# Kernel optimization log

Measured on AMD Instinct MI355X. Metric: run time of the kernel, lower is better.

The kernel has to match this reference:

```python
import jax, jax.numpy as jnp
import numpy as np

BS = 16
CIN = 32          # input_channels
COUT = 64         # out_channels
OUT_DIM = 1024    # out_dim
S = 2
S0 = 1
K = S * (S0 + 1)  # non-overlapping patch size = 4
D = OUT_DIM * K   # input spatial length = 4096


def setup_inputs() -> dict:
    key = jax.random.key(0)
    k1, k2 = jax.random.split(key)
    x = jax.random.normal(k1, (BS, CIN, D), dtype=jnp.float32)
    # learned parameter, torch.randn init
    weight = jax.random.normal(k2, (COUT, CIN, D), dtype=jnp.float32)
    return {"x": x, "weight": weight}


def reference(x, weight):
    # sharing == 0 path of NonOverlappingLocallyConnected1d:
    #   out[b,o,p] = (1/sqrt(CIN)) * sum_{c,k} x[b,c,p*K+k] * weight[o,c,p*K+k]
    # Original materializes [bs,cout,cin,D] via broadcast multiply then sums
    # over (cin, K); fused here as a single einsum over non-overlapping patches.
    bs = x.shape[0]
    xr = x.reshape(bs, CIN, OUT_DIM, K)        # [b, c, p, k]
    wr = weight.reshape(COUT, CIN, OUT_DIM, K)  # [o, c, p, k]
    out = jnp.einsum('bcpk,ocpk->bop', xr, wr)  # [b, o, p]
    return out / jnp.sqrt(jnp.asarray(CIN, x.dtype))
```

## Files before the change

### kernel.cpp

```cpp
#include <hip/hip_runtime.h>

#define BS      16
#define CIN     32
#define COUT    64
#define OUT_DIM 1024
#define PK      4
#define DD      4096

__global__ __launch_bounds__(256, 2) void nolc1d_kernel(
    const float* __restrict__ x,
    const float* __restrict__ w,
    float* __restrict__ out)
{
    const int t   = threadIdx.x;
    const int bid = blockIdx.x;
    const int gg  = bid & 255;
    const int oh  = bid >> 8;

    __shared__ float xs[BS * CIN * 16];
    float4* xs4 = (float4*)xs;

    const float4* __restrict__ x4p = (const float4*)x;
    #pragma unroll
    for (int l = 0; l < 8; ++l) {
        int idx  = t + l * 256;
        int pair = idx >> 2;
        int i    = idx & 3;
        int b    = pair >> 5;
        int c    = pair & 31;
        xs4[idx] = x4p[(size_t)b * (CIN * DD / 4) + c * (DD / 4) + gg * 4 + i];
    }
    __syncthreads();

    const int p_local = t & 3;
    const int o_idx   = (t >> 2) & 15;
    const int b0      = (t >> 6) * 4;
    const int o0      = oh * 32 + o_idx * 2;

    const float4* __restrict__ w4p = (const float4*)w;
    const size_t wstride_o = CIN * DD / 4;
    size_t wbase0 = (size_t)o0 * wstride_o + gg * 4 + p_local;
    size_t wbase1 = wbase0 + wstride_o;

    float acc[4][2] = {};

    #pragma unroll 8
    for (int c = 0; c < CIN; ++c) {
        float4 wv0 = w4p[wbase0 + (size_t)c * (DD / 4)];
        float4 wv1 = w4p[wbase1 + (size_t)c * (DD / 4)];
        #pragma unroll
        for (int bi = 0; bi < 4; ++bi) {
            float4 xv = xs4[((b0 + bi) * CIN + c) * 4 + p_local];
            acc[bi][0] += xv.x * wv0.x + xv.y * wv0.y + xv.z * wv0.z + xv.w * wv0.w;
            acc[bi][1] += xv.x * wv1.x + xv.y * wv1.y + xv.z * wv1.z + xv.w * wv1.w;
        }
    }

    const float scale = 0.17677669529663687f;
    const int pg = gg * 4 + p_local;
    #pragma unroll
    for (int bi = 0; bi < 4; ++bi) {
        #pragma unroll
        for (int j = 0; j < 2; ++j) {
            out[(size_t)(b0 + bi) * (COUT * OUT_DIM) +
                (size_t)(o0 + j) * OUT_DIM + pg] = acc[bi][j] * scale;
        }
    }
}

extern "C" void kernel_launch(void* const* d_in, const int* in_sizes, int n_in,
                              void* d_out, int out_size, void* d_ws, size_t ws_size,
                              hipStream_t stream) {
    const float* x = (const float*)d_in[0];
    const float* w = (const float*)d_in[1];
    float* out = (float*)d_out;

    nolc1d_kernel<<<dim3(512), dim3(256), 0, stream>>>(x, w, out);
}
```

Baseline: 91.19 us.

## Drop shared-memory x staging, split batch across blocks, remap blocks per XCD

Removes the LDS staging of x and the barrier; each thread now loads x directly from global memory and computes a 2x2 (batch x out-channel) tile instead of 4x2. The grid doubles to 1024 blocks by splitting batch into halves. Block indices are remapped so that blocks sharing a patch group land on the same XCD, which should let L2 serve repeated x and w reads. Occupancy hint rises to 4 blocks/SM. The cost is more redundant global and L2 traffic for x and w in exchange for more parallelism and fewer registers.

```diff
diff --git a/kernel.cpp b/kernel.cpp
--- a/kernel.cpp
+++ b/kernel.cpp
@@ -4,68 +4,60 @@
 #define CIN     32
 #define COUT    64
 #define OUT_DIM 1024
-#define PK      4
 #define DD      4096
 
-__global__ __launch_bounds__(256, 2) void nolc1d_kernel(
+__global__ __launch_bounds__(256, 4) void nolc1d_kernel(
     const float* __restrict__ x,
     const float* __restrict__ w,
     float* __restrict__ out)
 {
     const int t   = threadIdx.x;
     const int bid = blockIdx.x;
-    const int gg  = bid & 255;
-    const int oh  = bid >> 8;
 
-    __shared__ float xs[BS * CIN * 16];
-    float4* xs4 = (float4*)xs;
-
-    const float4* __restrict__ x4p = (const float4*)x;
-    #pragma unroll
-    for (int l = 0; l < 8; ++l) {
-        int idx  = t + l * 256;
-        int pair = idx >> 2;
-        int i    = idx & 3;
-        int b    = pair >> 5;
-        int c    = pair & 31;
-        xs4[idx] = x4p[(size_t)b * (CIN * DD / 4) + c * (DD / 4) + gg * 4 + i];
-    }
-    __syncthreads();
+    const int xcd = bid >> 7;
+    const int i   = bid & 127;
+    const int sub = i >> 5;
+    const int gg  = xcd * 32 + (i & 31);
+    const int oh  = sub & 1;
+    const int bh  = sub >> 1;
 
     const int p_local = t & 3;
     const int o_idx   = (t >> 2) & 15;
-    const int b0      = (t >> 6) * 4;
-    const int o0      = oh * 32 + o_idx * 2;
+    const int bg      = t >> 6;
 
-    const float4* __restrict__ w4p = (const float4*)w;
-    const size_t wstride_o = CIN * DD / 4;
-    size_t wbase0 = (size_t)o0 * wstride_o + gg * 4 + p_local;
-    size_t wbase1 = wbase0 + wstride_o;
+    const int o0 = oh * 32 + o_idx * 2;
+    const int b0 = bh * 8 + bg * 2;
 
-    float acc[4][2] = {};
+    const float4* __restrict__ x4 = (const float4*)x;
+    const float4* __restrict__ w4 = (const float4*)w;
 
-    #pragma unroll 8
+    const int rs = DD / 4;
+    const size_t xbase0 = (size_t)b0 * (CIN * rs) + gg * 4 + p_local;
+    const size_t xbase1 = xbase0 + (size_t)(CIN * rs);
+    const size_t wbase0 = (size_t)o0 * (CIN * rs) + gg * 4 + p_local;
+    const size_t wbase1 = wbase0 + (size_t)(CIN * rs);
+
+    float a00 = 0.f, a01 = 0.f, a10 = 0.f, a11 = 0.f;
+
+    #pragma unroll 4
     for (int c = 0; c < CIN; ++c) {
-        float4 wv0 = w4p[wbase0 + (size_t)c * (DD / 4)];
-        float4 wv1 = w4p[wbase1 + (size_t)c * (DD / 4)];
-        #pragma unroll
-        for (int bi = 0; bi < 4; ++bi) {
-            float4 xv = xs4[((b0 + bi) * CIN + c) * 4 + p_local];
-            acc[bi][0] += xv.x * wv0.x + xv.y * wv0.y + xv.z * wv0.z + xv.w * wv0.w;
-            acc[bi][1] += xv.x * wv1.x + xv.y * wv1.y + xv.z * wv1.z + xv.w * wv1.w;
-        }
+        float4 wv0 = w4[wbase0 + (size_t)c * rs];
+        float4 wv1 = w4[wbase1 + (size_t)c * rs];
+        float4 xv0 = x4[xbase0 + (size_t)c * rs];
+        float4 xv1 = x4[xbase1 + (size_t)c * rs];
+
+        a00 += xv0.x * wv0.x + xv0.y * wv0.y + xv0.z * wv0.z + xv0.w * wv0.w;
+        a01 += xv0.x * wv1.x + xv0.y * wv1.y + xv0.z * wv1.z + xv0.w * wv1.w;
+        a10 += xv1.x * wv0.x + xv1.y * wv0.y + xv1.z * wv0.z + xv1.w * wv0.w;
+        a11 += xv1.x * wv1.x + xv1.y * wv1.y + xv1.z * wv1.z + xv1.w * wv1.w;
     }
 
     const float scale = 0.17677669529663687f;
     const int pg = gg * 4 + p_local;
-    #pragma unroll
-    for (int bi = 0; bi < 4; ++bi) {
-        #pragma unroll
-        for (int j = 0; j < 2; ++j) {
-            out[(size_t)(b0 + bi) * (COUT * OUT_DIM) +
-                (size_t)(o0 + j) * OUT_DIM + pg] = acc[bi][j] * scale;
-        }
-    }
+    out[((size_t)b0       * COUT + o0    ) * OUT_DIM + pg] = a00 * scale;
+    out[((size_t)b0       * COUT + o0 + 1) * OUT_DIM + pg] = a01 * scale;
+    out[((size_t)(b0 + 1) * COUT + o0    ) * OUT_DIM + pg] = a10 * scale;
+    out[((size_t)(b0 + 1) * COUT + o0 + 1) * OUT_DIM + pg] = a11 * scale;
 }
 
 extern "C" void kernel_launch(void* const* d_in, const int* in_sizes, int n_in,
@@ -75,5 +67,5 @@
     const float* w = (const float*)d_in[1];
     float* out = (float*)d_out;
 
-    nolc1d_kernel<<<dim3(512), dim3(256), 0, stream>>>(x, w, out);
+    nolc1d_kernel<<<dim3(1024), dim3(256), 0, stream>>>(x, w, out);
 }
```

Measured after the change: 103.3 us. 1.13x slower.

## Retile over output channels and positions with double-buffered weight staging in LDS

Applied to the files above, without the earlier changes.

Reorganizes the kernel so each block owns 4 output channels and 64 patch positions. The block's weight slice is staged into shared memory in double-buffered chunks of 8 input channels, while x is read directly from global memory per wave. Block indices are swizzled so neighbouring position groups are spread across XCDs. The intent is wider, coalesced 64-lane float4 accesses and overlap of the weight fetch with compute. The trade-off is that x is now re-read from global/L2 by each of the 16 channel-group blocks, and the launch drops to 256 blocks of 512 threads, which may lower occupancy.

```diff
diff --git a/kernel.cpp b/kernel.cpp
--- a/kernel.cpp
+++ b/kernel.cpp
@@ -4,66 +4,82 @@
 #define CIN     32
 #define COUT    64
 #define OUT_DIM 1024
-#define PK      4
 #define DD      4096
 
-__global__ __launch_bounds__(256, 2) void nolc1d_kernel(
+#define OT      4
+#define PT      64
+#define CCH     8
+#define NCH     (CIN / CCH)
+
+__global__ __launch_bounds__(512, 2) void nolc1d_kernel(
     const float* __restrict__ x,
     const float* __restrict__ w,
     float* __restrict__ out)
 {
-    const int t   = threadIdx.x;
     const int bid = blockIdx.x;
-    const int gg  = bid & 255;
-    const int oh  = bid >> 8;
+    const int xcd = bid & 7;
+    const int j   = bid >> 3;
+    const int og  = j & 15;
+    const int pg  = xcd + 8 * (j >> 4);
+    const int o0  = og * OT;
+    const int p0  = pg * PT;
 
-    __shared__ float xs[BS * CIN * 16];
-    float4* xs4 = (float4*)xs;
+    const int t    = threadIdx.x;
+    const int lane = t & 63;
+    const int wv   = t >> 6;
+    const int b0   = wv * 2;
 
-    const float4* __restrict__ x4p = (const float4*)x;
-    #pragma unroll
-    for (int l = 0; l < 8; ++l) {
-        int idx  = t + l * 256;
-        int pair = idx >> 2;
-        int i    = idx & 3;
-        int b    = pair >> 5;
-        int c    = pair & 31;
-        xs4[idx] = x4p[(size_t)b * (CIN * DD / 4) + c * (DD / 4) + gg * 4 + i];
-    }
+    __shared__ float4 ws4[2][CCH * OT * 64];
+
+    const float4* __restrict__ x4 = (const float4*)x;
+    const float4* __restrict__ w4 = (const float4*)w;
+    const int rs = DD / 4;
+
+    auto stage = [&](int buf, int ch) {
+        #pragma unroll
+        for (int i = 0; i < 4; ++i) {
+            const int r    = wv * 4 + i;
+            const int c_in = r >> 2;
+            const int o_in = r & 3;
+            const int c    = ch * CCH + c_in;
+            ws4[buf][r * 64 + lane] =
+                w4[((size_t)(o0 + o_in) * CIN + c) * rs + p0 + lane];
+        }
+    };
+
+    float acc[2][OT] = {};
+
+    stage(0, 0);
     __syncthreads();
 
-    const int p_local = t & 3;
-    const int o_idx   = (t >> 2) & 15;
-    const int b0      = (t >> 6) * 4;
-    const int o0      = oh * 32 + o_idx * 2;
+    for (int ch = 0; ch < NCH; ++ch) {
+        if (ch + 1 < NCH) stage((ch + 1) & 1, ch + 1);
+        const int buf = ch & 1;
 
-    const float4* __restrict__ w4p = (const float4*)w;
-    const size_t wstride_o = CIN * DD / 4;
-    size_t wbase0 = (size_t)o0 * wstride_o + gg * 4 + p_local;
-    size_t wbase1 = wbase0 + wstride_o;
-
-    float acc[4][2] = {};
-
-    #pragma unroll 8
-    for (int c = 0; c < CIN; ++c) {
-        float4 wv0 = w4p[wbase0 + (size_t)c * (DD / 4)];
-        float4 wv1 = w4p[wbase1 + (size_t)c * (DD / 4)];
         #pragma unroll
-        for (int bi = 0; bi < 4; ++bi) {
-            float4 xv = xs4[((b0 + bi) * CIN + c) * 4 + p_local];
-            acc[bi][0] += xv.x * wv0.x + xv.y * wv0.y + xv.z * wv0.z + xv.w * wv0.w;
-            acc[bi][1] += xv.x * wv1.x + xv.y * wv1.y + xv.z * wv1.z + xv.w * wv1.w;
+        for (int ci = 0; ci < CCH; ++ci) {
+            const int c = ch * CCH + ci;
+            const float4 xv0 = x4[((size_t)b0       * CIN + c) * rs + p0 + lane];
+            const float4 xv1 = x4[((size_t)(b0 + 1) * CIN + c) * rs + p0 + lane];
+            #pragma unroll
+            for (int o = 0; o < OT; ++o) {
+                const float4 wvv = ws4[buf][(ci * OT + o) * 64 + lane];
+                acc[0][o] += xv0.x * wvv.x + xv0.y * wvv.y +
+                             xv0.z * wvv.z + xv0.w * wvv.w;
+                acc[1][o] += xv1.x * wvv.x + xv1.y * wvv.y +
+                             xv1.z * wvv.z + xv1.w * wvv.w;
+            }
         }
+        __syncthreads();
     }
 
     const float scale = 0.17677669529663687f;
-    const int pg = gg * 4 + p_local;
     #pragma unroll
-    for (int bi = 0; bi < 4; ++bi) {
+    for (int bi = 0; bi < 2; ++bi) {
         #pragma unroll
-        for (int j = 0; j < 2; ++j) {
-            out[(size_t)(b0 + bi) * (COUT * OUT_DIM) +
-                (size_t)(o0 + j) * OUT_DIM + pg] = acc[bi][j] * scale;
+        for (int o = 0; o < OT; ++o) {
+            out[((size_t)(b0 + bi) * COUT + (o0 + o)) * OUT_DIM + p0 + lane] =
+                acc[bi][o] * scale;
         }
     }
 }
@@ -75,5 +91,5 @@
     const float* w = (const float*)d_in[1];
     float* out = (float*)d_out;
 
-    nolc1d_kernel<<<dim3(512), dim3(256), 0, stream>>>(x, w, out);
+    nolc1d_kernel<<<dim3(256), dim3(512), 0, stream>>>(x, w, out);
 }
```

Result: faster. 89.14 us (-2.2%).
